# Optimization experiments

Measured on AMD Instinct MI355X. Metric: run time of the kernel, lower is better.

## Reference

```python
import jax, jax.numpy as jnp
import numpy as np

B, S, D, H = 2, 2048, 1024, 16
HD = D // H  # 64

def setup_inputs() -> dict:
    key = jax.random.key(0)
    ks = jax.random.split(key, 8)
    scale = 0.02
    return {
        "hidden_states": jax.random.normal(ks[0], (B, S, D), jnp.float32),
        "attention_mask": jnp.zeros((B, 1, 1, S), jnp.float32),
        "bias_matrix_chunk": jax.random.normal(ks[1], (S, S), jnp.float32),
        "bias_coef": jax.random.uniform(ks[2], (1,), jnp.float32),
        "Wq": jax.random.normal(ks[3], (D, D), jnp.float32) * scale,
        "bq": jnp.zeros((D,), jnp.float32),
        "Wk": jax.random.normal(ks[4], (D, D), jnp.float32) * scale,
        "bk": jnp.zeros((D,), jnp.float32),
        "Wv": jax.random.normal(ks[5], (D, D), jnp.float32) * scale,
        "bv": jnp.zeros((D,), jnp.float32),
    }

def reference(hidden_states, attention_mask, bias_matrix_chunk, bias_coef,
              Wq, bq, Wk, bk, Wv, bv):
    # q/k/v projections: [B,S,D] -> [B,H,S,HD]
    def heads(x):
        return x.reshape(B, S, H, HD).transpose(0, 2, 1, 3)
    q = heads(hidden_states @ Wq + bq)
    k = heads(hidden_states @ Wk + bk)
    v = heads(hidden_states @ Wv + bv)
    scores = jnp.einsum("bhqd,bhkd->bhqk", q, k) / jnp.sqrt(jnp.float32(HD))
    # custom additive bias, broadcast over batch and heads
    scores = scores + bias_matrix_chunk[None, None, :, :] * bias_coef[0]
    scores = scores + attention_mask  # additive mask [B,1,1,S]
    probs = jax.nn.softmax(scores, axis=-1)  # dropout prob 0 -> identity
    ctx = jnp.einsum("bhqk,bhkd->bhqd", probs, v)
    return ctx.transpose(0, 2, 1, 3).reshape(B, S, D)
```

## Files before the change

### kernel.cpp

```cpp
#include <hip/hip_runtime.h>

typedef unsigned short u16;
typedef __attribute__((ext_vector_type(8))) short bf16x8;
typedef __attribute__((ext_vector_type(4))) float f32x4;
typedef __attribute__((ext_vector_type(8))) unsigned short u16x8;
typedef __attribute__((ext_vector_type(4))) unsigned short u16x4;
typedef __attribute__((ext_vector_type(4))) float f32x4v;

#define LOG2E 1.4426950408889634f
#define QSCALE 0.18033688011112042f

#define SB 2048
#define DB 1024
#define NH 16
#define HD 64

__device__ __forceinline__ u16 f2bf(float f) {
  unsigned u = __float_as_uint(f);
  return (u16)((u + 0x7FFFu + ((u >> 16) & 1u)) >> 16);
}
__device__ __forceinline__ float bf2f(u16 h) {
  return __uint_as_float(((unsigned)h) << 16);
}
__device__ __forceinline__ unsigned cvt_pk_bf16(float lo, float hi) {
  unsigned r;
  asm("v_cvt_pk_bf16_f32 %0, %1, %2" : "=v"(r) : "v"(lo), "v"(hi));
  return r;
}

__device__ __forceinline__ void gload_lds16(const void* g, void* l) {
  __builtin_amdgcn_global_load_lds((const __attribute__((address_space(1))) void*)g,
                                   (__attribute__((address_space(3))) void*)l, 16, 0, 0);
}


__global__ void conv_x_kernel(const float* __restrict__ in, u16* __restrict__ out) {
  int i = blockIdx.x * blockDim.x + threadIdx.x;
  const f32x4v* p = (const f32x4v*)in + (size_t)i * 2;
  f32x4v a = p[0], b = p[1];
  u16x8 o;
  o[0] = f2bf(a[0]); o[1] = f2bf(a[1]); o[2] = f2bf(a[2]); o[3] = f2bf(a[3]);
  o[4] = f2bf(b[0]); o[5] = f2bf(b[1]); o[6] = f2bf(b[2]); o[7] = f2bf(b[3]);
  *((u16x8*)out + i) = o;
}

__global__ void conv_wt_kernel(const float* __restrict__ Wq, const float* __restrict__ Wk,
                               const float* __restrict__ Wv, u16* __restrict__ Wt) {
  __shared__ float tile[32][33];
  int z = blockIdx.z;
  const float* W = (z == 0) ? Wq : (z == 1) ? Wk : Wv;
  int k0 = blockIdx.x * 32, n0 = blockIdx.y * 32;
  int tx = threadIdx.x;
  for (int i = threadIdx.y; i < 32; i += 8)
    tile[i][tx] = W[(size_t)(k0 + i) * DB + n0 + tx];
  __syncthreads();
  for (int i = threadIdx.y; i < 32; i += 8)
    Wt[(size_t)z * DB * DB + (size_t)(n0 + i) * DB + k0 + tx] = f2bf(tile[tx][i]);
}

__global__ __launch_bounds__(256) void conv_biasr_kernel(
    const float* __restrict__ biasM, const float* __restrict__ coef,
    const float* __restrict__ mask, u16* __restrict__ biasR) {
  __shared__ float tile[64 * 64];
  __shared__ float msh[64];
  int ktb = blockIdx.x, q64b = blockIdx.y, b = blockIdx.z;
  int q0 = q64b * 64, k0 = ktb * 64;
  int tid = threadIdx.x;
  float c = coef[0] * LOG2E;
  for (int i = tid; i < 4096; i += 256)
    tile[i] = biasM[(size_t)(q0 + (i >> 6)) * SB + k0 + (i & 63)];
  if (tid < 64) msh[tid] = mask[b * SB + k0 + tid] * LOG2E;
  __syncthreads();
  int wid = tid >> 6, lane = tid & 63, lrow = lane & 15, lk = lane >> 4;
  int qloc = wid * 16 + lrow;
  u16x8 o0, o1;
#pragma unroll
  for (int e = 0; e < 16; e++) {
    int kloc = (e >> 2) * 16 + lk * 4 + (e & 3);
    float v = tile[qloc * 64 + kloc] * c + msh[kloc];
    if (e < 8) o0[e] = f2bf(v); else o1[e - 8] = f2bf(v);
  }
  int widp = (q64b & 1) * 4 + wid;
  size_t base = ((((size_t)b * 16 + (q64b >> 1)) * 32 + ktb) * 8 + widp) * 1024 + lane * 16;
  *(u16x8*)&biasR[base] = o0;
  *(u16x8*)&biasR[base + 8] = o1;
}

__global__ __launch_bounds__(256) void gemm_qk_kernel(
    const u16* __restrict__ X, const u16* __restrict__ Wt,
    const float* __restrict__ bq, const float* __restrict__ bk,
    u16* __restrict__ Q, u16* __restrict__ K) {
  __shared__ __align__(16) u16 As[128 * 32];
  __shared__ __align__(16) u16 Bs[128 * 32];
  int z = blockIdx.z;
  const u16* Wz = Wt + (size_t)z * DB * DB;
  const float* bias = (z == 0) ? bq : bk;
  u16* dst = (z == 0) ? Q : K;
  int m0 = blockIdx.x * 128, n0 = blockIdx.y * 128;
  int tid = threadIdx.x, wid = tid >> 6, lane = tid & 63;
  int wr = wid >> 1, wc = wid & 1;
  int lrow = lane & 15, lk = lane >> 4;
  int srow = lane >> 2, scol = (lane & 3) * 8;

  f32x4 acc[4][4];
#pragma unroll
  for (int i = 0; i < 4; i++)
#pragma unroll
    for (int j = 0; j < 4; j++) acc[i][j] = (f32x4){0.f, 0.f, 0.f, 0.f};

  for (int k0 = 0; k0 < DB; k0 += 32) {
#pragma unroll
    for (int p = 0; p < 2; p++) {
      int c = p * 4 + wid;
      gload_lds16(X + (size_t)(m0 + c * 16 + srow) * DB + k0 + scol, &As[c * 512]);
      gload_lds16(Wz + (size_t)(n0 + c * 16 + srow) * DB + k0 + scol, &Bs[c * 512]);
    }
    __syncthreads();
    bf16x8 af[4], bf_[4];
#pragma unroll
    for (int i = 0; i < 4; i++)
      af[i] = *(const bf16x8*)&As[(wr * 64 + i * 16 + lrow) * 32 + lk * 8];
#pragma unroll
    for (int j = 0; j < 4; j++)
      bf_[j] = *(const bf16x8*)&Bs[(wc * 64 + j * 16 + lrow) * 32 + lk * 8];
#pragma unroll
    for (int i = 0; i < 4; i++)
#pragma unroll
      for (int j = 0; j < 4; j++)
        acc[i][j] = __builtin_amdgcn_mfma_f32_16x16x32_bf16(bf_[j], af[i], acc[i][j], 0, 0, 0);
    __syncthreads();
  }

  int h = (n0 >> 6) + wc;
#pragma unroll
  for (int j = 0; j < 4; j++) {
    int nb = wc * 64 + j * 16 + lk * 4;
    f32x4v bb4 = *(const f32x4v*)&bias[n0 + nb];
    int hd0 = nb & 63;
#pragma unroll
    for (int i = 0; i < 4; i++) {
      int m = m0 + wr * 64 + i * 16 + lrow;
      int b = m >> 11, s = m & (SB - 1);
      int bh = b * NH + h;
      u16x4 pk;
      if (z == 0) {
#pragma unroll
        for (int r = 0; r < 4; r++) pk[r] = f2bf((acc[i][j][r] + bb4[r]) * QSCALE);
        *(u16x4*)&dst[((size_t)bh * SB + s) * HD + hd0] = pk;
      } else {
#pragma unroll
        for (int r = 0; r < 4; r++) pk[r] = f2bf(acc[i][j][r] + bb4[r]);
        *(u16x4*)&dst[((size_t)bh * SB + s) * HD + (hd0 ^ ((s & 7) << 3))] = pk;
      }
    }
  }
}

__global__ __launch_bounds__(256) void gemm_v_kernel(
    const u16* __restrict__ X, const u16* __restrict__ Wt,
    const float* __restrict__ bv, u16* __restrict__ V) {
  __shared__ __align__(16) u16 As[128 * 32];
  __shared__ __align__(16) u16 Bs[128 * 32];
  const u16* Wz = Wt + (size_t)2 * DB * DB;
  int m0 = blockIdx.x * 128, n0 = blockIdx.y * 128;
  int tid = threadIdx.x, wid = tid >> 6, lane = tid & 63;
  int wr = wid >> 1, wc = wid & 1;
  int lrow = lane & 15, lk = lane >> 4;
  int srow = lane >> 2, scol = (lane & 3) * 8;

  f32x4 acc[4][4];
#pragma unroll
  for (int i = 0; i < 4; i++)
#pragma unroll
    for (int j = 0; j < 4; j++) acc[i][j] = (f32x4){0.f, 0.f, 0.f, 0.f};

  for (int k0 = 0; k0 < DB; k0 += 32) {
#pragma unroll
    for (int p = 0; p < 2; p++) {
      int c = p * 4 + wid;
      gload_lds16(X + (size_t)(m0 + c * 16 + srow) * DB + k0 + scol, &As[c * 512]);
      gload_lds16(Wz + (size_t)(n0 + c * 16 + srow) * DB + k0 + scol, &Bs[c * 512]);
    }
    __syncthreads();
    bf16x8 af[4], bf_[4];
#pragma unroll
    for (int i = 0; i < 4; i++)
      af[i] = *(const bf16x8*)&As[(wr * 64 + i * 16 + lrow) * 32 + lk * 8];
#pragma unroll
    for (int j = 0; j < 4; j++)
      bf_[j] = *(const bf16x8*)&Bs[(wc * 64 + j * 16 + lrow) * 32 + lk * 8];
#pragma unroll
    for (int i = 0; i < 4; i++)
#pragma unroll
      for (int j = 0; j < 4; j++)
        acc[i][j] = __builtin_amdgcn_mfma_f32_16x16x32_bf16(af[i], bf_[j], acc[i][j], 0, 0, 0);
    __syncthreads();
  }

#pragma unroll
  for (int j = 0; j < 4; j++) {
    int n = n0 + wc * 64 + j * 16 + lrow;
    float bb = bv[n];
    int h = n >> 6, hd = n & 63;
#pragma unroll
    for (int i = 0; i < 4; i++) {
      int mbase = m0 + wr * 64 + i * 16 + lk * 4;
      int b = mbase >> 11;
      int s = mbase & (SB - 1);
      int bh = b * NH + h;
      u16x4 pk;
#pragma unroll
      for (int r = 0; r < 4; r++) pk[r] = f2bf(acc[i][j][r] + bb);
      size_t idx = ((size_t)bh * HD + hd) * SB + (s & ~63) + ((s & 63) ^ ((hd & 7) << 3));
      *(u16x4*)&V[idx] = pk;
    }
  }
}

__global__ __launch_bounds__(512) void attn_kernel(
    const u16* __restrict__ Q, const u16* __restrict__ K, const u16* __restrict__ Vt,
    const u16* __restrict__ biasR, float* __restrict__ out) {
  __shared__ __align__(16) u16 Klds[2][4096];
  __shared__ __align__(16) u16 Vlds[2][4096];
  __shared__ __align__(16) u16 P[8][1024];
  int h = blockIdx.x;
  int b = blockIdx.y >> 4, q0b = blockIdx.y & 15;
  int bh = b * NH + h;
  int q0 = q0b * 128;
  int tid = threadIdx.x, wid = tid >> 6, lane = tid & 63;
  int lrow = lane & 15, lk = lane >> 4;
  const u16* Qb = Q + (size_t)bh * SB * HD;
  const u16* Kb = K + (size_t)bh * SB * HD;
  const u16* Vb = Vt + (size_t)bh * HD * SB;
  const u16* biasW = biasR + ((((size_t)b * 16 + q0b) * 32) * 8 + wid) * 1024 + lane * 16;

  int qr = q0 + wid * 16 + lrow;
  bf16x8 qf0 = *(const bf16x8*)&Qb[(size_t)qr * HD + lk * 8];
  bf16x8 qf1 = *(const bf16x8*)&Qb[(size_t)qr * HD + 32 + lk * 8];

  const bf16x8 vones = {0x3F80, 0x3F80, 0x3F80, 0x3F80, 0x3F80, 0x3F80, 0x3F80, 0x3F80};

  int kst = wid * 512 + lane * 8;
  int vrow_st = wid * 8 + (lane >> 3), vslot = lane & 7;

  f32x4 acc[4], accl;
#pragma unroll
  for (int d = 0; d < 4; d++) acc[d] = (f32x4){0.f, 0.f, 0.f, 0.f};
  accl = (f32x4){0.f, 0.f, 0.f, 0.f};
  u16* Pw = &P[wid][0];

  gload_lds16(Kb + kst, &Klds[0][wid * 512]);
  gload_lds16(Vb + (size_t)vrow_st * SB + vslot * 8, &Vlds[0][wid * 512]);
  u16x8 bc0 = *(const u16x8*)biasW;
  u16x8 bc1 = *(const u16x8*)(biasW + 8);
  __syncthreads();

#pragma unroll 2
  for (int ktb = 0; ktb < 32; ktb++) {
    int cur = ktb & 1;
    if (ktb < 31) {
      int ktn = (ktb + 1) * 64;
      gload_lds16(Kb + (size_t)ktn * HD + kst, &Klds[cur ^ 1][wid * 512]);
      gload_lds16(Vb + (size_t)vrow_st * SB + ktn + vslot * 8, &Vlds[cur ^ 1][wid * 512]);
    }
    int ktp = (ktb + 1) & 31;
    u16x8 bn0 = *(const u16x8*)(biasW + (size_t)ktp * 8192);
    u16x8 bn1 = *(const u16x8*)(biasW + (size_t)ktp * 8192 + 8);

    f32x4 bf[4];
#pragma unroll
    for (int kb = 0; kb < 4; kb++)
#pragma unroll
      for (int r = 0; r < 4; r++) {
        int e = kb * 4 + r;
        bf[kb][r] = bf2f(e < 8 ? bc0[e] : bc1[e - 8]);
      }

    f32x4 s[4];
    __builtin_amdgcn_s_setprio(1);
#pragma unroll
    for (int kb = 0; kb < 4; kb++) {
      int krow = kb * 16 + lrow;
      int sw = (krow & 7) << 3;
      bf16x8 ka0 = *(const bf16x8*)&Klds[cur][krow * 64 + ((lk * 8) ^ sw)];
      bf16x8 ka1 = *(const bf16x8*)&Klds[cur][krow * 64 + ((32 + lk * 8) ^ sw)];
      f32x4 t = __builtin_amdgcn_mfma_f32_16x16x32_bf16(ka0, qf0, bf[kb], 0, 0, 0);
      s[kb] = __builtin_amdgcn_mfma_f32_16x16x32_bf16(ka1, qf1, t, 0, 0, 0);
    }
    __builtin_amdgcn_s_setprio(0);

#pragma unroll
    for (int kb = 0; kb < 4; kb++) {
      float pv0 = exp2f(s[kb][0]), pv1 = exp2f(s[kb][1]);
      float pv2 = exp2f(s[kb][2]), pv3 = exp2f(s[kb][3]);
      unsigned d0 = cvt_pk_bf16(pv0, pv1);
      unsigned d1 = cvt_pk_bf16(pv2, pv3);
      int byte = (lrow * 128 + kb * 32 + lk * 8) ^ ((lrow & 7) << 4);
      *(uint2*)((char*)Pw + byte) = make_uint2(d0, d1);
    }
    bc0 = bn0; bc1 = bn1;
    asm volatile("s_waitcnt lgkmcnt(0)" ::: "memory");

    bf16x8 pa[2];
#pragma unroll
    for (int ks = 0; ks < 2; ks++) {
      int byte = (lrow * 128 + ks * 64 + lk * 16) ^ ((lrow & 7) << 4);
      pa[ks] = *(const bf16x8*)((char*)Pw + byte);
    }
    __builtin_amdgcn_s_setprio(1);
    accl = __builtin_amdgcn_mfma_f32_16x16x32_bf16(pa[0], vones, accl, 0, 0, 0);
    accl = __builtin_amdgcn_mfma_f32_16x16x32_bf16(pa[1], vones, accl, 0, 0, 0);
#pragma unroll
    for (int db = 0; db < 4; db++) {
      int vrow = db * 16 + lrow;
      int sw = (vrow & 7) << 3;
#pragma unroll
      for (int ks = 0; ks < 2; ks++) {
        bf16x8 vb = *(const bf16x8*)&Vlds[cur][vrow * 64 + ((ks * 32 + lk * 8) ^ sw)];
        acc[db] = __builtin_amdgcn_mfma_f32_16x16x32_bf16(pa[ks], vb, acc[db], 0, 0, 0);
      }
    }
    __builtin_amdgcn_s_setprio(0);
    __syncthreads();
  }

  float inv[4];
#pragma unroll
  for (int r = 0; r < 4; r++) inv[r] = 1.0f / accl[r];
#pragma unroll
  for (int db = 0; db < 4; db++) {
#pragma unroll
    for (int r = 0; r < 4; r++) {
      int qg = q0 + wid * 16 + lk * 4 + r;
      out[((size_t)b * SB + qg) * DB + h * HD + db * 16 + lrow] = acc[db][r] * inv[r];
    }
  }
}

extern "C" void kernel_launch(void* const* d_in, const int* in_sizes, int n_in,
                              void* d_out, int out_size, void* d_ws, size_t ws_size,
                              hipStream_t stream) {
  const float* hs    = (const float*)d_in[0];
  const float* mask  = (const float*)d_in[1];
  const float* biasM = (const float*)d_in[2];
  const float* coef  = (const float*)d_in[3];
  const float* Wq    = (const float*)d_in[4];
  const float* bq    = (const float*)d_in[5];
  const float* Wk    = (const float*)d_in[6];
  const float* bk    = (const float*)d_in[7];
  const float* Wv    = (const float*)d_in[8];
  const float* bv    = (const float*)d_in[9];
  float* out = (float*)d_out;

  char* w = (char*)d_ws;
  u16* Qb    = (u16*)(w);
  u16* Kb    = (u16*)(w + 8u * 1024 * 1024);
  u16* Vb    = (u16*)(w + 16u * 1024 * 1024);
  u16* X     = (u16*)(w + 24u * 1024 * 1024);
  u16* Wt    = (u16*)(w + 32u * 1024 * 1024);
  u16* biasR = (u16*)(w + 24u * 1024 * 1024);

  conv_x_kernel<<<2048, 256, 0, stream>>>(hs, X);
  conv_wt_kernel<<<dim3(32, 32, 3), dim3(32, 8), 0, stream>>>(Wq, Wk, Wv, Wt);
  gemm_qk_kernel<<<dim3(32, 8, 2), 256, 0, stream>>>(X, Wt, bq, bk, Qb, Kb);
  gemm_v_kernel<<<dim3(32, 8, 1), 256, 0, stream>>>(X, Wt, bv, Vb);
  conv_biasr_kernel<<<dim3(32, 32, 2), 256, 0, stream>>>(biasM, coef, mask, biasR);
  attn_kernel<<<dim3(NH, 32), 512, 0, stream>>>(Qb, Kb, Vb, biasR, out);
}
```

Before: 227.2 us.

## Merge QKV projection GEMMs into one launch and hand-pipeline attention loop

The separate Q/K and V projection kernels become a single launch with a z dimension of 3, branching on z for the V layout. This removes one kernel launch and lets all 768 tiles share the GPU at once. The attention loop is manually unrolled into two macro phases with explicit double-buffer indices and ping-pong bias registers. The full __syncthreads is replaced by s_waitcnt vmcnt(2) plus s_barrier and a sched_barrier, so next-tile loads can stay in flight across the barrier. The partial vmcnt wait relies on exact counting of outstanding loads, which is fragile if the compiler reorders memory ops.

```diff
diff --git a/kernel.cpp b/kernel.cpp
--- a/kernel.cpp
+++ b/kernel.cpp
@@ -86,16 +86,14 @@
   *(u16x8*)&biasR[base + 8] = o1;
 }
 
-__global__ __launch_bounds__(256) void gemm_qk_kernel(
+__global__ __launch_bounds__(256) void gemm_qkv_kernel(
     const u16* __restrict__ X, const u16* __restrict__ Wt,
-    const float* __restrict__ bq, const float* __restrict__ bk,
-    u16* __restrict__ Q, u16* __restrict__ K) {
+    const float* __restrict__ bq, const float* __restrict__ bk, const float* __restrict__ bv,
+    u16* __restrict__ Q, u16* __restrict__ K, u16* __restrict__ V) {
   __shared__ __align__(16) u16 As[128 * 32];
   __shared__ __align__(16) u16 Bs[128 * 32];
   int z = blockIdx.z;
   const u16* Wz = Wt + (size_t)z * DB * DB;
-  const float* bias = (z == 0) ? bq : bk;
-  u16* dst = (z == 0) ? Q : K;
   int m0 = blockIdx.x * 128, n0 = blockIdx.y * 128;
   int tid = threadIdx.x, wid = tid >> 6, lane = tid & 63;
   int wr = wid >> 1, wc = wid & 1;
@@ -108,114 +106,160 @@
 #pragma unroll
     for (int j = 0; j < 4; j++) acc[i][j] = (f32x4){0.f, 0.f, 0.f, 0.f};
 
-  for (int k0 = 0; k0 < DB; k0 += 32) {
-#pragma unroll
-    for (int p = 0; p < 2; p++) {
-      int c = p * 4 + wid;
-      gload_lds16(X + (size_t)(m0 + c * 16 + srow) * DB + k0 + scol, &As[c * 512]);
-      gload_lds16(Wz + (size_t)(n0 + c * 16 + srow) * DB + k0 + scol, &Bs[c * 512]);
-    }
-    __syncthreads();
-    bf16x8 af[4], bf_[4];
-#pragma unroll
-    for (int i = 0; i < 4; i++)
-      af[i] = *(const bf16x8*)&As[(wr * 64 + i * 16 + lrow) * 32 + lk * 8];
-#pragma unroll
-    for (int j = 0; j < 4; j++)
-      bf_[j] = *(const bf16x8*)&Bs[(wc * 64 + j * 16 + lrow) * 32 + lk * 8];
-#pragma unroll
-    for (int i = 0; i < 4; i++)
+  if (z < 2) {
+    for (int k0 = 0; k0 < DB; k0 += 32) {
+#pragma unroll
+      for (int p = 0; p < 2; p++) {
+        int c = p * 4 + wid;
+        gload_lds16(X + (size_t)(m0 + c * 16 + srow) * DB + k0 + scol, &As[c * 512]);
+        gload_lds16(Wz + (size_t)(n0 + c * 16 + srow) * DB + k0 + scol, &Bs[c * 512]);
+      }
+      __syncthreads();
+      bf16x8 af[4], bf_[4];
+#pragma unroll
+      for (int i = 0; i < 4; i++)
+        af[i] = *(const bf16x8*)&As[(wr * 64 + i * 16 + lrow) * 32 + lk * 8];
 #pragma unroll
       for (int j = 0; j < 4; j++)
-        acc[i][j] = __builtin_amdgcn_mfma_f32_16x16x32_bf16(bf_[j], af[i], acc[i][j], 0, 0, 0);
-    __syncthreads();
-  }
-
-  int h = (n0 >> 6) + wc;
-#pragma unroll
-  for (int j = 0; j < 4; j++) {
-    int nb = wc * 64 + j * 16 + lk * 4;
-    f32x4v bb4 = *(const f32x4v*)&bias[n0 + nb];
-    int hd0 = nb & 63;
-#pragma unroll
-    for (int i = 0; i < 4; i++) {
-      int m = m0 + wr * 64 + i * 16 + lrow;
-      int b = m >> 11, s = m & (SB - 1);
-      int bh = b * NH + h;
-      u16x4 pk;
-      if (z == 0) {
-#pragma unroll
-        for (int r = 0; r < 4; r++) pk[r] = f2bf((acc[i][j][r] + bb4[r]) * QSCALE);
-        *(u16x4*)&dst[((size_t)bh * SB + s) * HD + hd0] = pk;
-      } else {
-#pragma unroll
-        for (int r = 0; r < 4; r++) pk[r] = f2bf(acc[i][j][r] + bb4[r]);
-        *(u16x4*)&dst[((size_t)bh * SB + s) * HD + (hd0 ^ ((s & 7) << 3))] = pk;
+        bf_[j] = *(const bf16x8*)&Bs[(wc * 64 + j * 16 + lrow) * 32 + lk * 8];
+#pragma unroll
+      for (int i = 0; i < 4; i++)
+#pragma unroll
+        for (int j = 0; j < 4; j++)
+          acc[i][j] = __builtin_amdgcn_mfma_f32_16x16x32_bf16(bf_[j], af[i], acc[i][j], 0, 0, 0);
+      __syncthreads();
+    }
+    const float* bias = (z == 0) ? bq : bk;
+    u16* dst = (z == 0) ? Q : K;
+    int h = (n0 >> 6) + wc;
+#pragma unroll
+    for (int j = 0; j < 4; j++) {
+      int nb = wc * 64 + j * 16 + lk * 4;
+      f32x4v bb4 = *(const f32x4v*)&bias[n0 + nb];
+      int hd0 = nb & 63;
+#pragma unroll
+      for (int i = 0; i < 4; i++) {
+        int m = m0 + wr * 64 + i * 16 + lrow;
+        int b = m >> 11, s = m & (SB - 1);
+        int bh = b * NH + h;
+        u16x4 pk;
+        if (z == 0) {
+#pragma unroll
+          for (int r = 0; r < 4; r++) pk[r] = f2bf((acc[i][j][r] + bb4[r]) * QSCALE);
+          *(u16x4*)&dst[((size_t)bh * SB + s) * HD + hd0] = pk;
+        } else {
+#pragma unroll
+          for (int r = 0; r < 4; r++) pk[r] = f2bf(acc[i][j][r] + bb4[r]);
+          *(u16x4*)&dst[((size_t)bh * SB + s) * HD + (hd0 ^ ((s & 7) << 3))] = pk;
+        }
       }
     }
-  }
-}
-
-__global__ __launch_bounds__(256) void gemm_v_kernel(
-    const u16* __restrict__ X, const u16* __restrict__ Wt,
-    const float* __restrict__ bv, u16* __restrict__ V) {
-  __shared__ __align__(16) u16 As[128 * 32];
-  __shared__ __align__(16) u16 Bs[128 * 32];
-  const u16* Wz = Wt + (size_t)2 * DB * DB;
-  int m0 = blockIdx.x * 128, n0 = blockIdx.y * 128;
-  int tid = threadIdx.x, wid = tid >> 6, lane = tid & 63;
-  int wr = wid >> 1, wc = wid & 1;
-  int lrow = lane & 15, lk = lane >> 4;
-  int srow = lane >> 2, scol = (lane & 3) * 8;
-
-  f32x4 acc[4][4];
-#pragma unroll
-  for (int i = 0; i < 4; i++)
-#pragma unroll
-    for (int j = 0; j < 4; j++) acc[i][j] = (f32x4){0.f, 0.f, 0.f, 0.f};
-
-  for (int k0 = 0; k0 < DB; k0 += 32) {
-#pragma unroll
-    for (int p = 0; p < 2; p++) {
-      int c = p * 4 + wid;
-      gload_lds16(X + (size_t)(m0 + c * 16 + srow) * DB + k0 + scol, &As[c * 512]);
-      gload_lds16(Wz + (size_t)(n0 + c * 16 + srow) * DB + k0 + scol, &Bs[c * 512]);
-    }
-    __syncthreads();
-    bf16x8 af[4], bf_[4];
-#pragma unroll
-    for (int i = 0; i < 4; i++)
-      af[i] = *(const bf16x8*)&As[(wr * 64 + i * 16 + lrow) * 32 + lk * 8];
-#pragma unroll
-    for (int j = 0; j < 4; j++)
-      bf_[j] = *(const bf16x8*)&Bs[(wc * 64 + j * 16 + lrow) * 32 + lk * 8];
-#pragma unroll
-    for (int i = 0; i < 4; i++)
+  } else {
+    for (int k0 = 0; k0 < DB; k0 += 32) {
+#pragma unroll
+      for (int p = 0; p < 2; p++) {
+        int c = p * 4 + wid;
+        gload_lds16(X + (size_t)(m0 + c * 16 + srow) * DB + k0 + scol, &As[c * 512]);
+        gload_lds16(Wz + (size_t)(n0 + c * 16 + srow) * DB + k0 + scol, &Bs[c * 512]);
+      }
+      __syncthreads();
+      bf16x8 af[4], bf_[4];
+#pragma unroll
+      for (int i = 0; i < 4; i++)
+        af[i] = *(const bf16x8*)&As[(wr * 64 + i * 16 + lrow) * 32 + lk * 8];
 #pragma unroll
       for (int j = 0; j < 4; j++)
-        acc[i][j] = __builtin_amdgcn_mfma_f32_16x16x32_bf16(af[i], bf_[j], acc[i][j], 0, 0, 0);
-    __syncthreads();
-  }
-
-#pragma unroll
-  for (int j = 0; j < 4; j++) {
-    int n = n0 + wc * 64 + j * 16 + lrow;
-    float bb = bv[n];
-    int h = n >> 6, hd = n & 63;
-#pragma unroll
-    for (int i = 0; i < 4; i++) {
-      int mbase = m0 + wr * 64 + i * 16 + lk * 4;
-      int b = mbase >> 11;
-      int s = mbase & (SB - 1);
-      int bh = b * NH + h;
-      u16x4 pk;
-#pragma unroll
-      for (int r = 0; r < 4; r++) pk[r] = f2bf(acc[i][j][r] + bb);
-      size_t idx = ((size_t)bh * HD + hd) * SB + (s & ~63) + ((s & 63) ^ ((hd & 7) << 3));
-      *(u16x4*)&V[idx] = pk;
-    }
-  }
-}
+        bf_[j] = *(const bf16x8*)&Bs[(wc * 64 + j * 16 + lrow) * 32 + lk * 8];
+#pragma unroll
+      for (int i = 0; i < 4; i++)
+#pragma unroll
+        for (int j = 0; j < 4; j++)
+          acc[i][j] = __builtin_amdgcn_mfma_f32_16x16x32_bf16(af[i], bf_[j], acc[i][j], 0, 0, 0);
+      __syncthreads();
+    }
+#pragma unroll
+    for (int j = 0; j < 4; j++) {
+      int n = n0 + wc * 64 + j * 16 + lrow;
+      float bb = bv[n];
+      int h = n >> 6, hd = n & 63;
+#pragma unroll
+      for (int i = 0; i < 4; i++) {
+        int mbase = m0 + wr * 64 + i * 16 + lk * 4;
+        int b = mbase >> 11;
+        int s = mbase & (SB - 1);
+        int bh = b * NH + h;
+        u16x4 pk;
+#pragma unroll
+        for (int r = 0; r < 4; r++) pk[r] = f2bf(acc[i][j][r] + bb);
+        size_t idx = ((size_t)bh * HD + hd) * SB + (s & ~63) + ((s & 63) ^ ((hd & 7) << 3));
+        *(u16x4*)&V[idx] = pk;
+      }
+    }
+  }
+}
+
+
+#define ATTN_PHASE(CUR, KTB, C0, C1, N0, N1)                                          \
+  {                                                                                   \
+    int ktb_ = (KTB);                                                                 \
+    int kt_ = ktb_ * 64;                                                              \
+    if (ktb_ < 31) {                                                                  \
+      gload_lds16(Kb + (size_t)(kt_ + 64) * HD + kst, &Klds[(CUR) ^ 1][wid * 512]);   \
+      gload_lds16(Vb + (size_t)vrow_st * SB + kt_ + 64 + vslot * 8,                   \
+                  &Vlds[(CUR) ^ 1][wid * 512]);                                       \
+    }                                                                                 \
+    int ktp_ = (ktb_ + 1) & 31;                                                       \
+    N0 = *(const u16x8*)(biasW + (size_t)ktp_ * 8192);                                \
+    N1 = *(const u16x8*)(biasW + (size_t)ktp_ * 8192 + 8);                            \
+    f32x4 bf_[4];                                                                     \
+    _Pragma("unroll") for (int kb = 0; kb < 4; kb++)                                  \
+        _Pragma("unroll") for (int r = 0; r < 4; r++) {                               \
+      int e = kb * 4 + r;                                                             \
+      bf_[kb][r] = bf2f(e < 8 ? C0[e] : C1[e - 8]);                                   \
+    }                                                                                 \
+    f32x4 s_[4];                                                                      \
+    __builtin_amdgcn_s_setprio(1);                                                    \
+    _Pragma("unroll") for (int kb = 0; kb < 4; kb++) {                                \
+      int krow = kb * 16 + lrow;                                                      \
+      int sw = (krow & 7) << 3;                                                       \
+      bf16x8 ka0 = *(const bf16x8*)&Klds[CUR][krow * 64 + ((lk * 8) ^ sw)];           \
+      bf16x8 ka1 = *(const bf16x8*)&Klds[CUR][krow * 64 + ((32 + lk * 8) ^ sw)];      \
+      f32x4 t_ = __builtin_amdgcn_mfma_f32_16x16x32_bf16(ka0, qf0, bf_[kb], 0, 0, 0); \
+      s_[kb] = __builtin_amdgcn_mfma_f32_16x16x32_bf16(ka1, qf1, t_, 0, 0, 0);        \
+    }                                                                                 \
+    __builtin_amdgcn_s_setprio(0);                                                    \
+    _Pragma("unroll") for (int kb = 0; kb < 4; kb++) {                                \
+      float pv0 = exp2f(s_[kb][0]), pv1 = exp2f(s_[kb][1]);                           \
+      float pv2 = exp2f(s_[kb][2]), pv3 = exp2f(s_[kb][3]);                           \
+      unsigned d0 = cvt_pk_bf16(pv0, pv1);                                            \
+      unsigned d1 = cvt_pk_bf16(pv2, pv3);                                            \
+      int byte = (lrow * 128 + kb * 32 + lk * 8) ^ ((lrow & 7) << 4);                 \
+      *(uint2*)((char*)Pw + byte) = make_uint2(d0, d1);                               \
+    }                                                                                 \
+    asm volatile("s_waitcnt lgkmcnt(0)" ::: "memory");                                \
+    bf16x8 pa0, pa1;                                                                  \
+    {                                                                                 \
+      int b0 = (lrow * 128 + lk * 16) ^ ((lrow & 7) << 4);                            \
+      int b1 = (lrow * 128 + 64 + lk * 16) ^ ((lrow & 7) << 4);                       \
+      pa0 = *(const bf16x8*)((char*)Pw + b0);                                         \
+      pa1 = *(const bf16x8*)((char*)Pw + b1);                                         \
+    }                                                                                 \
+    __builtin_amdgcn_s_setprio(1);                                                    \
+    accl = __builtin_amdgcn_mfma_f32_16x16x32_bf16(pa0, vones, accl, 0, 0, 0);        \
+    accl = __builtin_amdgcn_mfma_f32_16x16x32_bf16(pa1, vones, accl, 0, 0, 0);        \
+    _Pragma("unroll") for (int db = 0; db < 4; db++) {                                \
+      int vrow = db * 16 + lrow;                                                      \
+      int sw = (vrow & 7) << 3;                                                       \
+      bf16x8 vb0 = *(const bf16x8*)&Vlds[CUR][vrow * 64 + ((lk * 8) ^ sw)];           \
+      bf16x8 vb1 = *(const bf16x8*)&Vlds[CUR][vrow * 64 + ((32 + lk * 8) ^ sw)];      \
+      acc[db] = __builtin_amdgcn_mfma_f32_16x16x32_bf16(pa0, vb0, acc[db], 0, 0, 0);  \
+      acc[db] = __builtin_amdgcn_mfma_f32_16x16x32_bf16(pa1, vb1, acc[db], 0, 0, 0);  \
+    }                                                                                 \
+    __builtin_amdgcn_s_setprio(0);                                                    \
+    asm volatile("s_waitcnt vmcnt(2)" ::: "memory");                                  \
+    __builtin_amdgcn_s_barrier();                                                     \
+    __builtin_amdgcn_sched_barrier(0);                                                \
+  }
 
 __global__ __launch_bounds__(512) void attn_kernel(
     const u16* __restrict__ Q, const u16* __restrict__ K, const u16* __restrict__ Vt,
@@ -251,77 +295,14 @@
 
   gload_lds16(Kb + kst, &Klds[0][wid * 512]);
   gload_lds16(Vb + (size_t)vrow_st * SB + vslot * 8, &Vlds[0][wid * 512]);
-  u16x8 bc0 = *(const u16x8*)biasW;
-  u16x8 bc1 = *(const u16x8*)(biasW + 8);
+  u16x8 bA0 = *(const u16x8*)biasW;
+  u16x8 bA1 = *(const u16x8*)(biasW + 8);
+  u16x8 bB0, bB1;
   __syncthreads();
 
-#pragma unroll 2
-  for (int ktb = 0; ktb < 32; ktb++) {
-    int cur = ktb & 1;
-    if (ktb < 31) {
-      int ktn = (ktb + 1) * 64;
-      gload_lds16(Kb + (size_t)ktn * HD + kst, &Klds[cur ^ 1][wid * 512]);
-      gload_lds16(Vb + (size_t)vrow_st * SB + ktn + vslot * 8, &Vlds[cur ^ 1][wid * 512]);
-    }
-    int ktp = (ktb + 1) & 31;
-    u16x8 bn0 = *(const u16x8*)(biasW + (size_t)ktp * 8192);
-    u16x8 bn1 = *(const u16x8*)(biasW + (size_t)ktp * 8192 + 8);
-
-    f32x4 bf[4];
-#pragma unroll
-    for (int kb = 0; kb < 4; kb++)
-#pragma unroll
-      for (int r = 0; r < 4; r++) {
-        int e = kb * 4 + r;
-        bf[kb][r] = bf2f(e < 8 ? bc0[e] : bc1[e - 8]);
-      }
-
-    f32x4 s[4];
-    __builtin_amdgcn_s_setprio(1);
-#pragma unroll
-    for (int kb = 0; kb < 4; kb++) {
-      int krow = kb * 16 + lrow;
-      int sw = (krow & 7) << 3;
-      bf16x8 ka0 = *(const bf16x8*)&Klds[cur][krow * 64 + ((lk * 8) ^ sw)];
-      bf16x8 ka1 = *(const bf16x8*)&Klds[cur][krow * 64 + ((32 + lk * 8) ^ sw)];
-      f32x4 t = __builtin_amdgcn_mfma_f32_16x16x32_bf16(ka0, qf0, bf[kb], 0, 0, 0);
-      s[kb] = __builtin_amdgcn_mfma_f32_16x16x32_bf16(ka1, qf1, t, 0, 0, 0);
-    }
-    __builtin_amdgcn_s_setprio(0);
-
-#pragma unroll
-    for (int kb = 0; kb < 4; kb++) {
-      float pv0 = exp2f(s[kb][0]), pv1 = exp2f(s[kb][1]);
-      float pv2 = exp2f(s[kb][2]), pv3 = exp2f(s[kb][3]);
-      unsigned d0 = cvt_pk_bf16(pv0, pv1);
-      unsigned d1 = cvt_pk_bf16(pv2, pv3);
-      int byte = (lrow * 128 + kb * 32 + lk * 8) ^ ((lrow & 7) << 4);
-      *(uint2*)((char*)Pw + byte) = make_uint2(d0, d1);
-    }
-    bc0 = bn0; bc1 = bn1;
-    asm volatile("s_waitcnt lgkmcnt(0)" ::: "memory");
-
-    bf16x8 pa[2];
-#pragma unroll
-    for (int ks = 0; ks < 2; ks++) {
-      int byte = (lrow * 128 + ks * 64 + lk * 16) ^ ((lrow & 7) << 4);
-      pa[ks] = *(const bf16x8*)((char*)Pw + byte);
-    }
-    __builtin_amdgcn_s_setprio(1);
-    accl = __builtin_amdgcn_mfma_f32_16x16x32_bf16(pa[0], vones, accl, 0, 0, 0);
-    accl = __builtin_amdgcn_mfma_f32_16x16x32_bf16(pa[1], vones, accl, 0, 0, 0);
-#pragma unroll
-    for (int db = 0; db < 4; db++) {
-      int vrow = db * 16 + lrow;
-      int sw = (vrow & 7) << 3;
-#pragma unroll
-      for (int ks = 0; ks < 2; ks++) {
-        bf16x8 vb = *(const bf16x8*)&Vlds[cur][vrow * 64 + ((ks * 32 + lk * 8) ^ sw)];
-        acc[db] = __builtin_amdgcn_mfma_f32_16x16x32_bf16(pa[ks], vb, acc[db], 0, 0, 0);
-      }
-    }
-    __builtin_amdgcn_s_setprio(0);
-    __syncthreads();
+  for (int it = 0; it < 16; ++it) {
+    ATTN_PHASE(0, it * 2, bA0, bA1, bB0, bB1);
+    ATTN_PHASE(1, it * 2 + 1, bB0, bB1, bA0, bA1);
   }
 
   float inv[4];
@@ -362,8 +343,7 @@
 
   conv_x_kernel<<<2048, 256, 0, stream>>>(hs, X);
   conv_wt_kernel<<<dim3(32, 32, 3), dim3(32, 8), 0, stream>>>(Wq, Wk, Wv, Wt);
-  gemm_qk_kernel<<<dim3(32, 8, 2), 256, 0, stream>>>(X, Wt, bq, bk, Qb, Kb);
-  gemm_v_kernel<<<dim3(32, 8, 1), 256, 0, stream>>>(X, Wt, bv, Vb);
+  gemm_qkv_kernel<<<dim3(32, 8, 3), 256, 0, stream>>>(X, Wt, bq, bk, bv, Qb, Kb, Vb);
   conv_biasr_kernel<<<dim3(32, 32, 2), 256, 0, stream>>>(biasM, coef, mask, biasR);
   attn_kernel<<<dim3(NH, 32), 512, 0, stream>>>(Qb, Kb, Vb, biasR, out);
 }
```

Measured after the change: 223.6 us. About the same (-1.6%).
